# Performance work log

Measured on AMD Instinct MI355X. Metric: run time of the kernel, lower is better.

Reference implementation:

```python
import jax, jax.numpy as jnp
import numpy as np
import math

B, C, K, P, STRIDE, ITERS = 32, 32, 3, 4, 2, 3
PSIZE = P * P
EPS = 1e-8
LN_2PI = math.log(2.0 * math.pi)


def setup_inputs() -> dict:
    key = jax.random.key(0)
    k1, k2, k3, k4 = jax.random.split(key, 4)
    x = jax.random.uniform(k1, (8, 16, 16, B * (PSIZE + 1)), dtype=jnp.float32)
    weights = jax.random.normal(k2, (1, K * K * B, C, P, P), dtype=jnp.float32)
    beta_u = jax.random.normal(k3, (C,), dtype=jnp.float32) * 0.1
    beta_a = jax.random.normal(k4, (C,), dtype=jnp.float32) * 0.1
    return {"x": x, "weights": weights, "beta_u": beta_u, "beta_a": beta_a}


def _add_patches(x):
    b, h, w, c = x.shape
    oh = ow = (h - K + 1) // STRIDE
    # same nested-list indexing as the torch code: idxs shape [K, oh]
    idxs = np.array([[h_idx + k_idx for h_idx in range(0, h - K + 1, STRIDE)]
                     for k_idx in range(K)])
    x = x[:, idxs, :, :]            # [b, K, oh, w, c]
    x = x[:, :, :, idxs, :]         # [b, K, oh, K, ow, c]
    x = jnp.transpose(x, (0, 1, 3, 2, 4, 5))  # [b, K, K, oh, ow, c]
    return x, oh, ow


def _m_step(a_in, r, v, beta_u, beta_a, inv_temp):
    # v: [n, Bk, C, psize]; a_in: [n, Bk, 1]; r: [n, Bk, C]
    n, Bk, Cc, psize = v.shape
    r = r * a_in
    r = r / (jnp.sum(r, axis=2, keepdims=True) + EPS)
    r_sum = jnp.sum(r, axis=1, keepdims=True)                 # [n,1,C]
    coeff = (r / (r_sum + EPS))[..., None]                    # [n,Bk,C,1]
    mu = jnp.sum(coeff * v, axis=1, keepdims=True)            # [n,1,C,psize]
    sigma_sq = jnp.sum(coeff * (v - mu) ** 2, axis=1, keepdims=True) + EPS
    sig = sigma_sq.reshape(n, Cc, psize)
    cost_h = (beta_u[:, None] + jnp.log(jnp.sqrt(sig))) * r_sum.reshape(n, Cc, 1)
    a_out = jax.nn.sigmoid(inv_temp * (beta_a - jnp.sum(cost_h, axis=2)))  # [n,C]
    return a_out, mu, sigma_sq


def _e_step(mu, sigma_sq, a_out, v):
    ln_p = (-(v - mu) ** 2 / (2.0 * sigma_sq)
            - jnp.log(jnp.sqrt(sigma_sq)) - 0.5 * LN_2PI)     # [n,Bk,C,psize]
    ln_ap = jnp.sum(ln_p, axis=3) + jnp.log(a_out)[:, None, :]
    return jax.nn.softmax(ln_ap, axis=2)


def _em_routing(v, a_in, beta_u, beta_a):
    n, Bk, Cc, psize = v.shape
    r = jnp.full((n, Bk, Cc), 1.0 / Cc, dtype=v.dtype)
    final_lambda = 0.01
    a_out = mu = None
    for it in range(ITERS):  # small fixed loop (3 iters)
        inv_temp = final_lambda * (1.0 - 0.95 ** (it + 1.0))
        a_out, mu, sigma_sq = _m_step(a_in, r, v, beta_u, beta_a, inv_temp)
        if it < ITERS - 1:
            r = _e_step(mu, sigma_sq, a_out, v)
    return mu, a_out


def reference(x, weights, beta_u, beta_a):
    b = x.shape[0]
    xp, oh, ow = _add_patches(x)                 # [b,K,K,oh,ow,544]
    p_in = xp[..., :B * PSIZE].reshape(b * oh * ow, K * K * B, PSIZE)
    a_in = xp[..., B * PSIZE:].reshape(b * oh * ow, K * K * B, 1)
    xv = p_in.reshape(-1, K * K * B, P, P)
    # torch: x.repeat(...,C,1,1) @ w.repeat(b,...) -> batched small matmul
    v = jnp.einsum('nbpq,bcqr->nbcpr', xv, weights[0]).reshape(
        b * oh * ow, K * K * B, C, PSIZE)
    mu, a_out = _em_routing(v, a_in, beta_u, beta_a)
    p_out = mu.reshape(b, oh, ow, C * PSIZE)
    a_o = a_out.reshape(b, oh, ow, C)
    return jnp.concatenate([p_out, a_o], axis=3)  # [b, 7, 7, 544]
```

## Files before the change

kernel.cpp:

```cpp
#include <hip/hip_runtime.h>
#include <math.h>

#define EPS 1e-8f
#define LN_2PI 1.8378770664093453f

__device__ __forceinline__ void redsum4(float& a, float& b, float& c, float& d) {
    #pragma unroll
    for (int off = 16; off >= 1; off >>= 1) {
        float ta = __shfl_xor(a, off);
        float tb = __shfl_xor(b, off);
        float tc = __shfl_xor(c, off);
        float td = __shfl_xor(d, off);
        a += ta; b += tb; c += tc; d += td;
    }
}

__global__ __launch_bounds__(256, 2)
void convcaps_em_kernel(const float* __restrict__ x,
                        const float* __restrict__ w,
                        const float* __restrict__ bu,
                        const float* __restrict__ ba,
                        float* __restrict__ out)
{
    __shared__ __align__(16) float sbuf[9 * 544];
    __shared__ __align__(16) float red[4][32][36];

    const int n = blockIdx.x;
    const int t = threadIdx.x;
    const int c = t & 31;
    const int g = t >> 5;
    const int wv = t >> 6;

    for (int idx = t; idx < 9 * 136; idx += 256) {
        const int s  = idx / 136;
        const int e4 = idx - s * 136;
        int cell = n * 9 + s;
        const int b  = cell / 441; cell -= b * 441;
        const int kh = cell / 147; cell -= kh * 147;
        const int kw = cell / 49;  cell -= kw * 49;
        const int i  = cell / 7;
        const int j  = cell - i * 7;
        const float4* src = reinterpret_cast<const float4*>(
            x + (size_t)(((b * 16 + 2 * i + kh) * 16) + 2 * j + kw) * 544);
        reinterpret_cast<float4*>(sbuf + s * 544)[e4] = src[e4];
    }
    __syncthreads();
    for (int idx = t; idx < 288; idx += 256) {
        float* ap = sbuf + (idx >> 5) * 544 + 512 + (idx & 31);
        const float a = *ap;
        *ap = a / (a + EPS);
    }
    __syncthreads();

    const float bu_c = bu[c];
    const float ba_c = ba[c];

    float iv[16], dd[16];
    float lapBase = 0.0f;
    #pragma unroll
    for (int p = 0; p < 16; ++p) { iv[p] = 0.0f; dd[p] = 0.0f; }

    #pragma unroll
    for (int it = 0; it < 3; ++it) {
        float pS0 = 0.0f, pS1[16], pS2[16];
        #pragma unroll
        for (int p = 0; p < 16; ++p) { pS1[p] = 0.0f; pS2[p] = 0.0f; }

        #pragma unroll 1
        for (int j = 0; j < 9; ++j) {
            const float* xb = sbuf + j * 544;

            float v[4][16], ff[4];
            #pragma unroll
            for (int u = 0; u < 4; ++u) {
                const int m = g + 8 * u;
                const float* xp = xb + m * 16;
                const float* wp = w + ((size_t)((j << 5) + m) * 32 + c) * 16;
                float xa[16], wf[16];
                #pragma unroll
                for (int q = 0; q < 4; ++q) {
                    float4 tx = reinterpret_cast<const float4*>(xp)[q];
                    float4 tw = reinterpret_cast<const float4*>(wp)[q];
                    xa[4*q] = tx.x; xa[4*q+1] = tx.y; xa[4*q+2] = tx.z; xa[4*q+3] = tx.w;
                    wf[4*q] = tw.x; wf[4*q+1] = tw.y; wf[4*q+2] = tw.z; wf[4*q+3] = tw.w;
                }
                #pragma unroll
                for (int p = 0; p < 4; ++p) {
                    #pragma unroll
                    for (int r = 0; r < 4; ++r) {
                        v[u][p*4+r] = fmaf(xa[p*4+3], wf[12+r],
                                      fmaf(xa[p*4+2], wf[8+r],
                                      fmaf(xa[p*4+1], wf[4+r], xa[p*4+0] * wf[r])));
                    }
                }
                ff[u] = xb[512 + m];
            }

            float rho[4];
            if (it == 0) {
                #pragma unroll
                for (int u = 0; u < 4; ++u) rho[u] = ff[u] * 0.03125f;
            } else {
                float e[4], z[4];
                #pragma unroll
                for (int u = 0; u < 4; ++u) {
                    float sA = 0.0f, sB = 0.0f;
                    #pragma unroll
                    for (int p = 0; p < 16; p += 2) {
                        sA = fmaf(fmaf(iv[p],   v[u][p],   dd[p]),   v[u][p],   sA);
                        sB = fmaf(fmaf(iv[p+1], v[u][p+1], dd[p+1]), v[u][p+1], sB);
                    }
                    e[u] = __expf(lapBase - (sA + sB));
                    z[u] = e[u];
                }
                redsum4(z[0], z[1], z[2], z[3]);
                #pragma unroll
                for (int u = 0; u < 4; ++u)
                    rho[u] = e[u] * __fdividef(ff[u], z[u]);
            }

            pS0 += (rho[0] + rho[1]) + (rho[2] + rho[3]);
            #pragma unroll
            for (int p = 0; p < 16; ++p) {
                #pragma unroll
                for (int u = 0; u < 4; ++u) {
                    const float rv = rho[u] * v[u][p];
                    pS1[p] += rv;
                    pS2[p] = fmaf(rv, v[u][p], pS2[p]);
                }
            }
        }

        pS0 += __shfl_xor(pS0, 32);
        #pragma unroll
        for (int p = 0; p < 16; ++p) {
            pS1[p] += __shfl_xor(pS1[p], 32);
            pS2[p] += __shfl_xor(pS2[p], 32);
        }
        if ((t & 32) == 0) {
            float* rp = &red[wv][c][0];
            #pragma unroll
            for (int q = 0; q < 4; ++q) {
                reinterpret_cast<float4*>(rp)[q] =
                    make_float4(pS1[4*q], pS1[4*q+1], pS1[4*q+2], pS1[4*q+3]);
                reinterpret_cast<float4*>(rp + 16)[q] =
                    make_float4(pS2[4*q], pS2[4*q+1], pS2[4*q+2], pS2[4*q+3]);
            }
            rp[32] = pS0;
        }
        __syncthreads();
        float S0 = 0.0f, S1[16], S2[16];
        #pragma unroll
        for (int p = 0; p < 16; ++p) { S1[p] = 0.0f; S2[p] = 0.0f; }
        #pragma unroll
        for (int kk = 0; kk < 4; ++kk) {
            const float* rp = &red[kk][c][0];
            #pragma unroll
            for (int q = 0; q < 4; ++q) {
                const float4 t1 = reinterpret_cast<const float4*>(rp)[q];
                const float4 t2 = reinterpret_cast<const float4*>(rp + 16)[q];
                S1[4*q]   += t1.x; S1[4*q+1] += t1.y; S1[4*q+2] += t1.z; S1[4*q+3] += t1.w;
                S2[4*q]   += t2.x; S2[4*q+1] += t2.y; S2[4*q+2] += t2.z; S2[4*q+3] += t2.w;
            }
            S0 += rp[32];
        }
        __syncthreads();

        const float inv = 1.0f / (S0 + EPS);
        float sumHalfLog = 0.0f;
        if (it < 2) {
            float Cq = 0.0f;
            #pragma unroll
            for (int p = 0; p < 16; ++p) {
                const float m_ = S1[p] * inv;
                const float sg = (S2[p] - 2.0f * m_ * S1[p] + m_ * m_ * S0) * inv + EPS;
                const float ivp = 0.5f / sg;
                iv[p] = ivp;
                dd[p] = -2.0f * m_ * ivp;
                Cq = fmaf(m_ * m_, ivp, Cq);
                sumHalfLog += 0.5f * __logf(sg);
            }
            const float cost = (16.0f * bu_c + sumHalfLog) * S0;
            const float itc = (it == 0) ? 5.0e-4f : 9.75e-4f;
            const float a_out_c = 1.0f / (1.0f + __expf(-(itc * (ba_c - cost))));
            lapBase = __logf(a_out_c) - sumHalfLog - 8.0f * LN_2PI - Cq;
        } else {
            float mu[16];
            #pragma unroll
            for (int p = 0; p < 16; ++p) {
                const float m_ = S1[p] * inv;
                const float sg = (S2[p] - 2.0f * m_ * S1[p] + m_ * m_ * S0) * inv + EPS;
                mu[p] = m_;
                sumHalfLog += 0.5f * __logf(sg);
            }
            const float cost = (16.0f * bu_c + sumHalfLog) * S0;
            const float a_out_c = 1.0f / (1.0f + __expf(-(1.42625e-3f * (ba_c - cost))));
            if (g == 0) {
                float* po = out + (size_t)n * 544 + c * 16;
                #pragma unroll
                for (int q = 0; q < 4; ++q) {
                    reinterpret_cast<float4*>(po)[q] =
                        make_float4(mu[4*q], mu[4*q+1], mu[4*q+2], mu[4*q+3]);
                }
                out[(size_t)n * 544 + 512 + c] = a_out_c;
            }
        }
    }
}

extern "C" void kernel_launch(void* const* d_in, const int* in_sizes, int n_in,
                              void* d_out, int out_size, void* d_ws, size_t ws_size,
                              hipStream_t stream) {
    const float* x  = (const float*)d_in[0];
    const float* w  = (const float*)d_in[1];
    const float* bu = (const float*)d_in[2];
    const float* ba = (const float*)d_in[3];
    float* out = (float*)d_out;
    convcaps_em_kernel<<<392, 256, 0, stream>>>(x, w, bu, ba, out);
}
```

Before: 70.28 us.

## Use packed FP32 FMA for vote math and prefetch next weight tile

Rewrites the per-capsule vote computation, E-step quadratic and moment accumulation with two-wide vector FMAs (v_pk_fma_f32) to halve the FP32 instruction count. It also software-pipelines the global weight loads, keeping the current weight tile in registers and issuing loads for the next j during compute. Both raise register pressure (16 extra float4 weights held live) under launch_bounds(256,2), which could cause spills or lower occupancy.

```diff
diff --git a/kernel.cpp b/kernel.cpp
--- a/kernel.cpp
+++ b/kernel.cpp
@@ -1,8 +1,15 @@
 #include <hip/hip_runtime.h>
 #include <math.h>
 
+typedef float v2f __attribute__((ext_vector_type(2)));
+
 #define EPS 1e-8f
 #define LN_2PI 1.8378770664093453f
+
+__device__ __forceinline__ v2f pkfma(v2f a, v2f b, v2f c) {
+    return __builtin_elementwise_fma(a, b, c);
+}
+__device__ __forceinline__ v2f splat2(float s) { return (v2f){s, s}; }
 
 __device__ __forceinline__ void redsum4(float& a, float& b, float& c, float& d) {
     #pragma unroll
@@ -55,45 +62,56 @@
     const float bu_c = bu[c];
     const float ba_c = ba[c];
 
-    float iv[16], dd[16];
+    const float* wbase = w + (size_t)(g * 32 + c) * 16;
+
+    float4 wb[4][4];
+    #pragma unroll
+    for (int u = 0; u < 4; ++u) {
+        const float4* p = reinterpret_cast<const float4*>(wbase + u * 4096);
+        wb[u][0] = p[0]; wb[u][1] = p[1]; wb[u][2] = p[2]; wb[u][3] = p[3];
+    }
+
+    v2f iv[8], dd[8];
     float lapBase = 0.0f;
     #pragma unroll
-    for (int p = 0; p < 16; ++p) { iv[p] = 0.0f; dd[p] = 0.0f; }
+    for (int i = 0; i < 8; ++i) { iv[i] = splat2(0.f); dd[i] = splat2(0.f); }
 
     #pragma unroll
     for (int it = 0; it < 3; ++it) {
-        float pS0 = 0.0f, pS1[16], pS2[16];
-        #pragma unroll
-        for (int p = 0; p < 16; ++p) { pS1[p] = 0.0f; pS2[p] = 0.0f; }
+        v2f pS1[8], pS2[8];
+        float pS0 = 0.0f;
+        #pragma unroll
+        for (int i = 0; i < 8; ++i) { pS1[i] = splat2(0.f); pS2[i] = splat2(0.f); }
 
         #pragma unroll 1
         for (int j = 0; j < 9; ++j) {
-            const float* xb = sbuf + j * 544;
-
-            float v[4][16], ff[4];
+            const float* xb  = sbuf + j * 544;
+            const float* wnx = wbase + (size_t)((j == 8) ? 0 : j + 1) * 16384;
+
+            v2f vv[4][8];
+            float ff[4];
             #pragma unroll
             for (int u = 0; u < 4; ++u) {
-                const int m = g + 8 * u;
-                const float* xp = xb + m * 16;
-                const float* wp = w + ((size_t)((j << 5) + m) * 32 + c) * 16;
-                float xa[16], wf[16];
-                #pragma unroll
-                for (int q = 0; q < 4; ++q) {
-                    float4 tx = reinterpret_cast<const float4*>(xp)[q];
-                    float4 tw = reinterpret_cast<const float4*>(wp)[q];
-                    xa[4*q] = tx.x; xa[4*q+1] = tx.y; xa[4*q+2] = tx.z; xa[4*q+3] = tx.w;
-                    wf[4*q] = tw.x; wf[4*q+1] = tw.y; wf[4*q+2] = tw.z; wf[4*q+3] = tw.w;
-                }
-                #pragma unroll
-                for (int p = 0; p < 4; ++p) {
-                    #pragma unroll
-                    for (int r = 0; r < 4; ++r) {
-                        v[u][p*4+r] = fmaf(xa[p*4+3], wf[12+r],
-                                      fmaf(xa[p*4+2], wf[8+r],
-                                      fmaf(xa[p*4+1], wf[4+r], xa[p*4+0] * wf[r])));
-                    }
-                }
-                ff[u] = xb[512 + m];
+                const float4* xp = reinterpret_cast<const float4*>(xb + (g + 8 * u) * 16);
+                const float4 x0 = xp[0], x1 = xp[1], x2 = xp[2], x3 = xp[3];
+                ff[u] = xb[512 + g + 8 * u];
+
+                const v2f w00 = {wb[u][0].x, wb[u][0].y}, w01 = {wb[u][0].z, wb[u][0].w};
+                const v2f w10 = {wb[u][1].x, wb[u][1].y}, w11 = {wb[u][1].z, wb[u][1].w};
+                const v2f w20 = {wb[u][2].x, wb[u][2].y}, w21 = {wb[u][2].z, wb[u][2].w};
+                const v2f w30 = {wb[u][3].x, wb[u][3].y}, w31 = {wb[u][3].z, wb[u][3].w};
+
+                vv[u][0] = pkfma(splat2(x0.w), w30, pkfma(splat2(x0.z), w20, pkfma(splat2(x0.y), w10, splat2(x0.x) * w00)));
+                vv[u][1] = pkfma(splat2(x0.w), w31, pkfma(splat2(x0.z), w21, pkfma(splat2(x0.y), w11, splat2(x0.x) * w01)));
+                vv[u][2] = pkfma(splat2(x1.w), w30, pkfma(splat2(x1.z), w20, pkfma(splat2(x1.y), w10, splat2(x1.x) * w00)));
+                vv[u][3] = pkfma(splat2(x1.w), w31, pkfma(splat2(x1.z), w21, pkfma(splat2(x1.y), w11, splat2(x1.x) * w01)));
+                vv[u][4] = pkfma(splat2(x2.w), w30, pkfma(splat2(x2.z), w20, pkfma(splat2(x2.y), w10, splat2(x2.x) * w00)));
+                vv[u][5] = pkfma(splat2(x2.w), w31, pkfma(splat2(x2.z), w21, pkfma(splat2(x2.y), w11, splat2(x2.x) * w01)));
+                vv[u][6] = pkfma(splat2(x3.w), w30, pkfma(splat2(x3.z), w20, pkfma(splat2(x3.y), w10, splat2(x3.x) * w00)));
+                vv[u][7] = pkfma(splat2(x3.w), w31, pkfma(splat2(x3.z), w21, pkfma(splat2(x3.y), w11, splat2(x3.x) * w01)));
+
+                const float4* p = reinterpret_cast<const float4*>(wnx + u * 4096);
+                wb[u][0] = p[0]; wb[u][1] = p[1]; wb[u][2] = p[2]; wb[u][3] = p[3];
             }
 
             float rho[4];
@@ -104,13 +122,11 @@
                 float e[4], z[4];
                 #pragma unroll
                 for (int u = 0; u < 4; ++u) {
-                    float sA = 0.0f, sB = 0.0f;
+                    v2f acc = splat2(0.f);
                     #pragma unroll
-                    for (int p = 0; p < 16; p += 2) {
-                        sA = fmaf(fmaf(iv[p],   v[u][p],   dd[p]),   v[u][p],   sA);
-                        sB = fmaf(fmaf(iv[p+1], v[u][p+1], dd[p+1]), v[u][p+1], sB);
-                    }
-                    e[u] = __expf(lapBase - (sA + sB));
+                    for (int i = 0; i < 8; ++i)
+                        acc = pkfma(pkfma(iv[i], vv[u][i], dd[i]), vv[u][i], acc);
+                    e[u] = __expf(lapBase - (acc.x + acc.y));
                     z[u] = e[u];
                 }
                 redsum4(z[0], z[1], z[2], z[3]);
@@ -121,30 +137,33 @@
 
             pS0 += (rho[0] + rho[1]) + (rho[2] + rho[3]);
             #pragma unroll
-            for (int p = 0; p < 16; ++p) {
-                #pragma unroll
-                for (int u = 0; u < 4; ++u) {
-                    const float rv = rho[u] * v[u][p];
-                    pS1[p] += rv;
-                    pS2[p] = fmaf(rv, v[u][p], pS2[p]);
+            for (int u = 0; u < 4; ++u) {
+                const v2f r2 = splat2(rho[u]);
+                #pragma unroll
+                for (int i = 0; i < 8; ++i) {
+                    const v2f rv = r2 * vv[u][i];
+                    pS1[i] += rv;
+                    pS2[i] = pkfma(rv, vv[u][i], pS2[i]);
                 }
             }
         }
 
         pS0 += __shfl_xor(pS0, 32);
         #pragma unroll
-        for (int p = 0; p < 16; ++p) {
-            pS1[p] += __shfl_xor(pS1[p], 32);
-            pS2[p] += __shfl_xor(pS2[p], 32);
+        for (int i = 0; i < 8; ++i) {
+            pS1[i].x += __shfl_xor(pS1[i].x, 32);
+            pS1[i].y += __shfl_xor(pS1[i].y, 32);
+            pS2[i].x += __shfl_xor(pS2[i].x, 32);
+            pS2[i].y += __shfl_xor(pS2[i].y, 32);
         }
         if ((t & 32) == 0) {
             float* rp = &red[wv][c][0];
             #pragma unroll
             for (int q = 0; q < 4; ++q) {
                 reinterpret_cast<float4*>(rp)[q] =
-                    make_float4(pS1[4*q], pS1[4*q+1], pS1[4*q+2], pS1[4*q+3]);
+                    make_float4(pS1[2*q].x, pS1[2*q].y, pS1[2*q+1].x, pS1[2*q+1].y);
                 reinterpret_cast<float4*>(rp + 16)[q] =
-                    make_float4(pS2[4*q], pS2[4*q+1], pS2[4*q+2], pS2[4*q+3]);
+                    make_float4(pS2[2*q].x, pS2[2*q].y, pS2[2*q+1].x, pS2[2*q+1].y);
             }
             rp[32] = pS0;
         }
@@ -167,18 +186,20 @@
         __syncthreads();
 
         const float inv = 1.0f / (S0 + EPS);
-        float sumHalfLog = 0.0f;
         if (it < 2) {
-            float Cq = 0.0f;
-            #pragma unroll
-            for (int p = 0; p < 16; ++p) {
-                const float m_ = S1[p] * inv;
-                const float sg = (S2[p] - 2.0f * m_ * S1[p] + m_ * m_ * S0) * inv + EPS;
-                const float ivp = 0.5f / sg;
-                iv[p] = ivp;
-                dd[p] = -2.0f * m_ * ivp;
-                Cq = fmaf(m_ * m_, ivp, Cq);
-                sumHalfLog += 0.5f * __logf(sg);
+            float Cq = 0.0f, sumHalfLog = 0.0f;
+            #pragma unroll
+            for (int i = 0; i < 8; ++i) {
+                const float ma = S1[2*i]   * inv;
+                const float mb = S1[2*i+1] * inv;
+                const float sga = (S2[2*i]   - 2.0f * ma * S1[2*i]   + ma * ma * S0) * inv + EPS;
+                const float sgb = (S2[2*i+1] - 2.0f * mb * S1[2*i+1] + mb * mb * S0) * inv + EPS;
+                const float iva = 0.5f / sga;
+                const float ivb = 0.5f / sgb;
+                iv[i] = (v2f){iva, ivb};
+                dd[i] = (v2f){-2.0f * ma * iva, -2.0f * mb * ivb};
+                Cq += ma * ma * iva + mb * mb * ivb;
+                sumHalfLog += 0.5f * (__logf(sga) + __logf(sgb));
             }
             const float cost = (16.0f * bu_c + sumHalfLog) * S0;
             const float itc = (it == 0) ? 5.0e-4f : 9.75e-4f;
@@ -186,6 +207,7 @@
             lapBase = __logf(a_out_c) - sumHalfLog - 8.0f * LN_2PI - Cq;
         } else {
             float mu[16];
+            float sumHalfLog = 0.0f;
             #pragma unroll
             for (int p = 0; p < 16; ++p) {
                 const float m_ = S1[p] * inv;
```

New measurement: 75.18 us. +7.0%, slower.
